# Optimization experiments

Measured on AMD Instinct MI355X. Metric: run time of the kernel, lower is better.

Reference implementation:

```python
import jax, jax.numpy as jnp
import numpy as np


def _local2d(x, weight, stride, padding):
    """Locally-connected 2D conv: per-output-location filters.
    x: [N, C, H, W], weight: [h_out, w_out, O, C, k, k].
    Returns [N, O, h_out, w_out].
    """
    h_out, w_out, O, C, k, _ = weight.shape
    if padding > 0:
        x = jnp.pad(x, ((0, 0), (0, 0), (padding, padding), (padding, padding)))
    # Gather all k x k windows at once (no python loop over locations).
    ih = (jnp.arange(h_out) * stride)[:, None] + jnp.arange(k)[None, :]  # [h_out, k]
    iw = (jnp.arange(w_out) * stride)[:, None] + jnp.arange(k)[None, :]  # [w_out, k]
    # patches: [N, C, h_out, w_out, k, k]
    patches = x[:, :, ih[:, None, :, None], iw[None, :, None, :]]
    # out[n,o,h,w] = sum_{c,p,q} weight[h,w,o,c,p,q] * patches[n,c,h,w,p,q]
    return jnp.einsum('hwocpq,nchwpq->nohw', weight, patches)


def setup_inputs() -> dict:
    key = jax.random.key(0)
    k1, k2 = jax.random.split(key)
    B, CAT, C, H, W = 32, 10, 32, 32, 32
    O, K, STRIDE, PAD = 64, 3, 1, 1
    h_out = (H + 2 * PAD - K) // STRIDE + 1
    w_out = (W + 2 * PAD - K) // STRIDE + 1
    x = jax.random.normal(k1, (B, CAT, C, H, W), dtype=jnp.float32)
    # init_local with first_layer=False, mono=False: std = 1/sqrt(0.5*C*K^2)
    std = 1.0 / np.sqrt(0.5 * C * K ** 2)
    weight = jax.random.normal(k2, (h_out, w_out, O, C, K, K), dtype=jnp.float32) * std
    bias = jnp.zeros((CAT, O, h_out, w_out), dtype=jnp.float32)
    return {"x": x, "weight": weight, "bias": bias}


def reference(x, weight, bias):
    STRIDE, PAD = 1, 1
    B, CAT = x.shape[:2]
    x_flat = x.reshape((B * CAT,) + x.shape[2:])            # [B*CAT, C, H, W]
    out_flat = _local2d(x_flat, weight, STRIDE, PAD)        # [B*CAT, O, h_out, w_out]
    out = out_flat.reshape((B, CAT) + out_flat.shape[1:])   # [B, CAT, O, h_out, w_out]
    return out + bias[None]
```

## Files before the change

kernel.cpp:

```cpp
#include <hip/hip_runtime.h>
#include <hip/hip_bf16.h>


typedef __attribute__((ext_vector_type(8))) short short8;
typedef __attribute__((ext_vector_type(4))) float f32x4;
typedef __attribute__((ext_vector_type(4))) unsigned short ushort4b;

#define XT_ELEMS 10485760
#define OUTS_OFF_BYTES 20972544

__device__ __forceinline__ unsigned short f2bf(float f) {
    __hip_bfloat16 b = __float2bfloat16(f);
    return __builtin_bit_cast(unsigned short, b);
}

__global__ __launch_bounds__(256) void VecLocal2d_xpose(const float* __restrict__ x,
                                                        unsigned short* __restrict__ xT) {
    __shared__ unsigned short tile[64][66];
    if (blockIdx.x == 0 && threadIdx.x < 192)
        reinterpret_cast<unsigned int*>(xT + XT_ELEMS)[threadIdx.x] = 0u;
    const int ib = blockIdx.x % 512;
    const int mb = blockIdx.x / 512;
    const int il = threadIdx.x & 63;
    const int t4 = threadIdx.x >> 6;
#pragma unroll
    for (int p = 0; p < 16; ++p) {
        const int ml = t4 + p * 4;
        const float v = x[(size_t)(mb * 64 + ml) * 32768 + ib * 64 + il];
        tile[ml][il] = f2bf(v);
    }
    __syncthreads();
#pragma unroll
    for (int p = 0; p < 16; ++p) {
        const int iw = t4 + p * 4;
        xT[(size_t)(ib * 64 + iw) * 320 + mb * 64 + il] = tile[il][iw];
    }
}

__global__ __launch_bounds__(256, 2) void VecLocal2d_main(const unsigned short* __restrict__ xT,
                                                          const float* __restrict__ weight,
                                                          float* __restrict__ out_s) {
    __shared__ unsigned short wLDS[64 * 296];
    __shared__ unsigned short pLDS[64 * 296];

    const int bid = blockIdx.x;
    const int s = bid >> 7;
    const int hg = bid & 127;
    const int h = hg >> 2;
    const int w = ((hg & 3) << 3) | s;
    const int loc = h * 32 + w;

    const int tid = threadIdx.x;
    const int lane = tid & 63;
    const int wave = tid >> 6;
    const int quad = lane >> 4;
    const int l16 = lane & 15;
    const int wm = wave >> 1, wn = wave & 1;

    const float* wg = weight + (size_t)loc * 18432;
#pragma unroll
    for (int i = 0; i < 18; ++i) {
        const int f4i = tid + i * 256;
        const float4 v = reinterpret_cast<const float4*>(wg)[f4i];
        const int o = f4i / 72;
        const int k4 = (f4i - o * 72) * 4;
        ushort4b u;
        u.x = f2bf(v.x); u.y = f2bf(v.y); u.z = f2bf(v.z); u.w = f2bf(v.w);
        *reinterpret_cast<ushort4b*>(&wLDS[o * 296 + k4]) = u;
    }

    int xoff[18][4];
#pragma unroll
    for (int j = 0; j < 18; ++j) {
        const int kq = wave + 4 * j;
#pragma unroll
        for (int ii = 0; ii < 4; ++ii) {
            const int k = kq * 4 + ii;
            const int c = k / 9;
            const int r9 = k - c * 9;
            const int yy = r9 / 3;
            const int q = r9 - yy * 3;
            const int y = h - 1 + yy;
            const int xc = w - 1 + q;
            const bool valid = ((unsigned)y < 32u) && ((unsigned)xc < 32u);
            const int off = valid ? ((c * 32 + y) * 32 + xc) * 320 : XT_ELEMS;
            xoff[j][ii] = off + lane;
        }
    }

    __syncthreads();

    short8 bfr[2][9];
#pragma unroll
    for (int tni = 0; tni < 2; ++tni) {
        const int o = (wn * 2 + tni) * 16 + l16;
#pragma unroll
        for (int kt = 0; kt < 9; ++kt)
            bfr[tni][kt] = *reinterpret_cast<const short8*>(&wLDS[o * 296 + kt * 32 + quad * 8]);
    }

    float* os = out_s + (size_t)loc * 20480;

    for (int mt = 0; mt < 5; ++mt) {
        const int mb = mt * 64;
        __syncthreads();
#pragma unroll
        for (int j = 0; j < 18; ++j) {
            ushort4b u;
            u.x = xT[xoff[j][0] + mb];
            u.y = xT[xoff[j][1] + mb];
            u.z = xT[xoff[j][2] + mb];
            u.w = xT[xoff[j][3] + mb];
            const int kq = wave + 4 * j;
            *reinterpret_cast<ushort4b*>(&pLDS[lane * 296 + kq * 4]) = u;
        }
        __syncthreads();

        f32x4 acc[2][2] = {};
#pragma unroll
        for (int kt = 0; kt < 9; ++kt) {
            const short8 a0 = *reinterpret_cast<const short8*>(
                &pLDS[((wm * 2 + 0) * 16 + l16) * 296 + kt * 32 + quad * 8]);
            const short8 a1 = *reinterpret_cast<const short8*>(
                &pLDS[((wm * 2 + 1) * 16 + l16) * 296 + kt * 32 + quad * 8]);
            acc[0][0] = __builtin_amdgcn_mfma_f32_16x16x32_bf16(a0, bfr[0][kt], acc[0][0], 0, 0, 0);
            acc[0][1] = __builtin_amdgcn_mfma_f32_16x16x32_bf16(a0, bfr[1][kt], acc[0][1], 0, 0, 0);
            acc[1][0] = __builtin_amdgcn_mfma_f32_16x16x32_bf16(a1, bfr[0][kt], acc[1][0], 0, 0, 0);
            acc[1][1] = __builtin_amdgcn_mfma_f32_16x16x32_bf16(a1, bfr[1][kt], acc[1][1], 0, 0, 0);
        }

#pragma unroll
        for (int tmi = 0; tmi < 2; ++tmi)
#pragma unroll
            for (int tni = 0; tni < 2; ++tni) {
                const int o = (wn * 2 + tni) * 16 + l16;
#pragma unroll
                for (int r = 0; r < 4; ++r) {
                    const int m = mb + (wm * 2 + tmi) * 16 + quad * 4 + r;
                    os[m * 64 + o] = acc[tmi][tni][r];
                }
            }
    }
}

__global__ __launch_bounds__(256) void VecLocal2d_outT(const float* __restrict__ out_s,
                                                       const float* __restrict__ bias,
                                                       float* __restrict__ out) {
    __shared__ float tile[64][65];
    const int m = blockIdx.x >> 4;
    const int loc0 = (blockIdx.x & 15) * 64;
    const int t = threadIdx.x;
    const float* src = out_s + (size_t)loc0 * 20480 + m * 64;
#pragma unroll
    for (int p = 0; p < 4; ++p) {
        const int idx = p * 256 + t;
        const int lr = idx >> 4;
        const int c4 = (idx & 15) * 4;
        const float4 v = *reinterpret_cast<const float4*>(src + (size_t)lr * 20480 + c4);
        tile[lr][c4 + 0] = v.x; tile[lr][c4 + 1] = v.y;
        tile[lr][c4 + 2] = v.z; tile[lr][c4 + 3] = v.w;
    }
    __syncthreads();
    const int cat = m % 10;
#pragma unroll
    for (int p = 0; p < 4; ++p) {
        const int idx = p * 256 + t;
        const int o = idx >> 4;
        const int l4 = (idx & 15) * 4;
        const float4 bv = *reinterpret_cast<const float4*>(
            bias + ((size_t)(cat * 64 + o)) * 1024 + loc0 + l4);
        float4 v;
        v.x = tile[l4 + 0][o] + bv.x;
        v.y = tile[l4 + 1][o] + bv.y;
        v.z = tile[l4 + 2][o] + bv.z;
        v.w = tile[l4 + 3][o] + bv.w;
        *reinterpret_cast<float4*>(out + ((size_t)(m * 64 + o)) * 1024 + loc0 + l4) = v;
    }
}

extern "C" void kernel_launch(void* const* d_in, const int* in_sizes, int n_in,
                              void* d_out, int out_size, void* d_ws, size_t ws_size,
                              hipStream_t stream) {
    const float* x = (const float*)d_in[0];
    const float* wgt = (const float*)d_in[1];
    const float* bias = (const float*)d_in[2];
    float* out = (float*)d_out;
    unsigned short* xT = (unsigned short*)d_ws;
    float* out_s = (float*)((char*)d_ws + OUTS_OFF_BYTES);

    VecLocal2d_xpose<<<2560, 256, 0, stream>>>(x, xT);
    VecLocal2d_main<<<1024, 256, 0, stream>>>(xT, wgt, out_s);
    VecLocal2d_outT<<<5120, 256, 0, stream>>>(out_s, bias, out);
}
```

Before: 247.5 us.

## Use spatial-major channel-minor input layout and feed MFMA directly from global memory

The transpose kernel now writes the input as [y*32+x][m][c] in bf16, so each 3x3 tap is a contiguous 32-channel slice. The main kernel reorders the weight K dimension to tap-major/channel-minor and loads MFMA A operands straight from global memory with 16-byte vector loads. This removes the per-tile scalar gather into the patch LDS buffer and its barriers. The smaller LDS footprint allows raising occupancy to 4 blocks per CU, but it relies on L2/cache reuse of the overlapping windows.

```diff
diff --git a/kernel.cpp b/kernel.cpp
--- a/kernel.cpp
+++ b/kernel.cpp
@@ -6,8 +6,9 @@
 typedef __attribute__((ext_vector_type(4))) float f32x4;
 typedef __attribute__((ext_vector_type(4))) unsigned short ushort4b;
 
-#define XT_ELEMS 10485760
-#define OUTS_OFF_BYTES 20972544
+#define XT2_ELEMS 10485760
+#define ZSLAB_ELEMS 10240
+#define OUTS_OFF_BYTES 20992000
 
 __device__ __forceinline__ unsigned short f2bf(float f) {
     __hip_bfloat16 b = __float2bfloat16(f);
@@ -15,33 +16,44 @@
 }
 
 __global__ __launch_bounds__(256) void VecLocal2d_xpose(const float* __restrict__ x,
-                                                        unsigned short* __restrict__ xT) {
-    __shared__ unsigned short tile[64][66];
-    if (blockIdx.x == 0 && threadIdx.x < 192)
-        reinterpret_cast<unsigned int*>(xT + XT_ELEMS)[threadIdx.x] = 0u;
-    const int ib = blockIdx.x % 512;
-    const int mb = blockIdx.x / 512;
-    const int il = threadIdx.x & 63;
-    const int t4 = threadIdx.x >> 6;
+                                                        unsigned short* __restrict__ xT2) {
+    __shared__ unsigned short tile[64][68];
+    if (blockIdx.x == 0) {
 #pragma unroll
-    for (int p = 0; p < 16; ++p) {
-        const int ml = t4 + p * 4;
-        const float v = x[(size_t)(mb * 64 + ml) * 32768 + ib * 64 + il];
-        tile[ml][il] = f2bf(v);
+        for (int j = 0; j < 20; ++j)
+            reinterpret_cast<unsigned int*>(xT2 + XT2_ELEMS)[threadIdx.x + j * 256] = 0u;
+    }
+    const int mcb = blockIdx.x >> 4;
+    const int yxb = blockIdx.x & 15;
+    const int t = threadIdx.x;
+    const int g = t >> 4;
+    const int l4 = (t & 15) * 4;
+#pragma unroll
+    for (int p = 0; p < 4; ++p) {
+        const int ml = g + p * 16;
+        const float4 v = *reinterpret_cast<const float4*>(
+            x + (size_t)(mcb * 64 + ml) * 1024 + yxb * 64 + l4);
+        ushort4b u;
+        u.x = f2bf(v.x); u.y = f2bf(v.y); u.z = f2bf(v.z); u.w = f2bf(v.w);
+        *reinterpret_cast<ushort4b*>(&tile[ml][l4]) = u;
     }
     __syncthreads();
 #pragma unroll
-    for (int p = 0; p < 16; ++p) {
-        const int iw = t4 + p * 4;
-        xT[(size_t)(ib * 64 + iw) * 320 + mb * 64 + il] = tile[il][iw];
+    for (int p = 0; p < 4; ++p) {
+        const int yl = g + p * 16;
+        ushort4b u;
+        u.x = tile[l4 + 0][yl];
+        u.y = tile[l4 + 1][yl];
+        u.z = tile[l4 + 2][yl];
+        u.w = tile[l4 + 3][yl];
+        *reinterpret_cast<ushort4b*>(xT2 + (size_t)(yxb * 64 + yl) * 10240 + mcb * 64 + l4) = u;
     }
 }
 
-__global__ __launch_bounds__(256, 2) void VecLocal2d_main(const unsigned short* __restrict__ xT,
+__global__ __launch_bounds__(256, 4) void VecLocal2d_main(const unsigned short* __restrict__ xT2,
                                                           const float* __restrict__ weight,
                                                           float* __restrict__ out_s) {
     __shared__ unsigned short wLDS[64 * 296];
-    __shared__ unsigned short pLDS[64 * 296];
 
     const int bid = blockIdx.x;
     const int s = bid >> 7;
@@ -63,30 +75,27 @@
         const int f4i = tid + i * 256;
         const float4 v = reinterpret_cast<const float4*>(wg)[f4i];
         const int o = f4i / 72;
-        const int k4 = (f4i - o * 72) * 4;
-        ushort4b u;
-        u.x = f2bf(v.x); u.y = f2bf(v.y); u.z = f2bf(v.z); u.w = f2bf(v.w);
-        *reinterpret_cast<ushort4b*>(&wLDS[o * 296 + k4]) = u;
+        const int kbase = (f4i - o * 72) * 4;
+        const float vv[4] = {v.x, v.y, v.z, v.w};
+#pragma unroll
+        for (int e = 0; e < 4; ++e) {
+            const int k = kbase + e;
+            const int c = k / 9;
+            const int r = k - c * 9;
+            wLDS[o * 296 + r * 32 + c] = f2bf(vv[e]);
+        }
     }
 
-    int xoff[18][4];
+    int base[9];
 #pragma unroll
-    for (int j = 0; j < 18; ++j) {
-        const int kq = wave + 4 * j;
+    for (int dy = 0; dy < 3; ++dy)
 #pragma unroll
-        for (int ii = 0; ii < 4; ++ii) {
-            const int k = kq * 4 + ii;
-            const int c = k / 9;
-            const int r9 = k - c * 9;
-            const int yy = r9 / 3;
-            const int q = r9 - yy * 3;
-            const int y = h - 1 + yy;
-            const int xc = w - 1 + q;
+        for (int dx = 0; dx < 3; ++dx) {
+            const int y = h - 1 + dy;
+            const int xc = w - 1 + dx;
             const bool valid = ((unsigned)y < 32u) && ((unsigned)xc < 32u);
-            const int off = valid ? ((c * 32 + y) * 32 + xc) * 320 : XT_ELEMS;
-            xoff[j][ii] = off + lane;
+            base[dy * 3 + dx] = valid ? (y * 32 + xc) * 10240 : XT2_ELEMS;
         }
-    }
 
     __syncthreads();
 
@@ -99,30 +108,16 @@
             bfr[tni][kt] = *reinterpret_cast<const short8*>(&wLDS[o * 296 + kt * 32 + quad * 8]);
     }
 
+    const int laneA = (wm * 32 + l16) * 32 + quad * 8;
     float* os = out_s + (size_t)loc * 20480;
 
     for (int mt = 0; mt < 5; ++mt) {
-        const int mb = mt * 64;
-        __syncthreads();
-#pragma unroll
-        for (int j = 0; j < 18; ++j) {
-            ushort4b u;
-            u.x = xT[xoff[j][0] + mb];
-            u.y = xT[xoff[j][1] + mb];
-            u.z = xT[xoff[j][2] + mb];
-            u.w = xT[xoff[j][3] + mb];
-            const int kq = wave + 4 * j;
-            *reinterpret_cast<ushort4b*>(&pLDS[lane * 296 + kq * 4]) = u;
-        }
-        __syncthreads();
-
+        const int moff = laneA + mt * 2048;
         f32x4 acc[2][2] = {};
 #pragma unroll
         for (int kt = 0; kt < 9; ++kt) {
-            const short8 a0 = *reinterpret_cast<const short8*>(
-                &pLDS[((wm * 2 + 0) * 16 + l16) * 296 + kt * 32 + quad * 8]);
-            const short8 a1 = *reinterpret_cast<const short8*>(
-                &pLDS[((wm * 2 + 1) * 16 + l16) * 296 + kt * 32 + quad * 8]);
+            const short8 a0 = *reinterpret_cast<const short8*>(xT2 + base[kt] + moff);
+            const short8 a1 = *reinterpret_cast<const short8*>(xT2 + base[kt] + moff + 512);
             acc[0][0] = __builtin_amdgcn_mfma_f32_16x16x32_bf16(a0, bfr[0][kt], acc[0][0], 0, 0, 0);
             acc[0][1] = __builtin_amdgcn_mfma_f32_16x16x32_bf16(a0, bfr[1][kt], acc[0][1], 0, 0, 0);
             acc[1][0] = __builtin_amdgcn_mfma_f32_16x16x32_bf16(a1, bfr[0][kt], acc[1][0], 0, 0, 0);
@@ -136,7 +131,7 @@
                 const int o = (wn * 2 + tni) * 16 + l16;
 #pragma unroll
                 for (int r = 0; r < 4; ++r) {
-                    const int m = mb + (wm * 2 + tmi) * 16 + quad * 4 + r;
+                    const int m = mt * 64 + (wm * 2 + tmi) * 16 + quad * 4 + r;
                     os[m * 64 + o] = acc[tmi][tni][r];
                 }
             }
@@ -185,10 +180,10 @@
     const float* wgt = (const float*)d_in[1];
     const float* bias = (const float*)d_in[2];
     float* out = (float*)d_out;
-    unsigned short* xT = (unsigned short*)d_ws;
+    unsigned short* xT2 = (unsigned short*)d_ws;
     float* out_s = (float*)((char*)d_ws + OUTS_OFF_BYTES);
 
-    VecLocal2d_xpose<<<2560, 256, 0, stream>>>(x, xT);
-    VecLocal2d_main<<<1024, 256, 0, stream>>>(xT, wgt, out_s);
+    VecLocal2d_xpose<<<2560, 256, 0, stream>>>(x, xT2);
+    VecLocal2d_main<<<1024, 256, 0, stream>>>(xT2, wgt, out_s);
     VecLocal2d_outT<<<5120, 256, 0, stream>>>(out_s, bias, out);
 }
```

Result: faster. 222.9 us (-9.9%).
